# Kernel optimization log

Measured on AMD Instinct MI355X. Metric: run time of the kernel, lower is better.

The kernel has to match this reference:

```python
import jax, jax.numpy as jnp
import numpy as np

N = 20000          # nodes
E = 320000         # edges (avg degree 16)
HID = 256          # hidden_size
HEADS = 8          # num_heads
HD = HID // HEADS  # head_dim = 32


def setup_inputs() -> dict:
    key = jax.random.key(0)
    ks = jax.random.split(key, 12)
    scale = 1.0 / np.sqrt(HID).astype(np.float32)
    def lin_w(k):
        return jax.random.normal(k, (HID, HID), jnp.float32) * scale
    def lin_b(k):
        return jax.random.normal(k, (HID,), jnp.float32) * 0.01
    return {
        "h":   jax.random.normal(ks[0], (N, HID), jnp.float32),
        "Wq": lin_w(ks[1]), "bq": lin_b(ks[2]),
        "Wk": lin_w(ks[3]), "bk": lin_b(ks[4]),
        "Wv": lin_w(ks[5]), "bv": lin_b(ks[6]),
        "Wo": lin_w(ks[7]), "bo": lin_b(ks[8]),
        "rows": jax.random.randint(ks[9],  (E,), 0, N),  # dst/query node of each edge
        "cols": jax.random.randint(ks[10], (E,), 0, N),  # src/key node of each edge
    }


def reference(h, Wq, bq, Wk, bk, Wv, bv, Wo, bo, rows, cols):
    n = h.shape[0]
    scaling = HD ** (-0.5)
    # projections; reshape exactly as torch: (N, head_dim, num_heads)
    q = ((h @ Wq) + bq).reshape(n, HD, HEADS) * scaling
    k = ((h @ Wk) + bk).reshape(n, HD, HEADS)
    v = ((h @ Wv) + bv).reshape(n, HD, HEADS)
    # bsddmm: per-edge, per-head score s[e,h] = sum_d q[rows[e],d,h] * k[cols[e],d,h]
    s = jnp.einsum("edh,edh->eh", q[rows], k[cols])  # [E, HEADS]
    # sparse row-wise softmax (over each row's edges)
    m = jax.ops.segment_max(s, rows, num_segments=n)          # [N, HEADS]
    e = jnp.exp(s - m[rows])                                   # [E, HEADS]
    z = jax.ops.segment_sum(e, rows, num_segments=n)           # [N, HEADS]
    attn = e / z[rows]                                          # [E, HEADS]
    # bspmm: out[i,d,h] = sum_{e: rows[e]=i} attn[e,h] * v[cols[e],d,h]
    out = jax.ops.segment_sum(attn[:, None, :] * v[cols], rows, num_segments=n)  # [N, HD, HEADS]
    return out.reshape(n, -1) @ Wo + bo
```

## Files before the change

### kernel.cpp

```cpp
#include <hip/hip_runtime.h>
#include <hip/hip_bf16.h>
#include <math.h>

#define NNODES 20000
#define NEDGES 320000

using f32x4 = __attribute__((ext_vector_type(4))) float;
using s16x8 = __attribute__((ext_vector_type(8))) short;
using u16x8 = __attribute__((ext_vector_type(8))) unsigned short;

__device__ __forceinline__ float bf2f(unsigned short u) {
    union { unsigned int i; float f; } c; c.i = ((unsigned int)u) << 16; return c.f;
}
__device__ __forceinline__ unsigned short f2bf(float f) {
    __hip_bfloat16 h = __float2bfloat16(f);
    return *reinterpret_cast<unsigned short*>(&h);
}
__device__ __forceinline__ u16x8 packA(const float4& x, const float4& y) {
    u16x8 u; u[0]=f2bf(x.x); u[1]=f2bf(x.y); u[2]=f2bf(x.z); u[3]=f2bf(x.w);
             u[4]=f2bf(y.x); u[5]=f2bf(y.y); u[6]=f2bf(y.z); u[7]=f2bf(y.w);
    return u;
}

__global__ __launch_bounds__(256) void prep_hist_k(
    const float* __restrict__ Wq, const float* __restrict__ bq,
    const float* __restrict__ Wk, const float* __restrict__ bk,
    const float* __restrict__ Wv, const float* __restrict__ bv,
    const float* __restrict__ Wo, const int* __restrict__ rows,
    unsigned short* __restrict__ wt, float* __restrict__ bp,
    int* __restrict__ counts)
{
    const int gid = blockIdx.x * 256 + threadIdx.x;
    const float SC = 0.17677669529663687f;
    if (gid < 262144) {
        const int mat = gid >> 16, r = gid & 65535;
        if (mat < 3) {
            const int k = r >> 8, c = r & 255;
            const int n_old = ((c & 31) << 3) | (c >> 5);
            const float* W = (mat == 0) ? Wq : (mat == 1) ? Wk : Wv;
            float val = W[k * 256 + n_old];
            if (mat == 0) val *= SC;
            wt[mat * 65536 + c * 256 + k] = f2bf(val);
        } else {
            const int c = r >> 8, n = r & 255;
            const int n_old = ((c & 31) << 3) | (c >> 5);
            wt[3 * 65536 + n * 256 + c] = f2bf(Wo[n_old * 256 + n]);
        }
    } else if (gid < 262912) {
        const int idx = gid - 262144;
        const int mat = idx >> 8, c = idx & 255;
        const int n_old = ((c & 31) << 3) | (c >> 5);
        const float* b = (mat == 0) ? bq : (mat == 1) ? bk : bv;
        float val = b[n_old];
        if (mat == 0) val *= SC;
        bp[mat * 256 + c] = val;
    } else if (gid < 262912 + NEDGES) {
        atomicAdd(&counts[rows[gid - 262912]], 1);
    }
}

__global__ __launch_bounds__(1024) void scan_k(const int* __restrict__ counts,
                                               int* __restrict__ row_start)
{
    __shared__ int wsum[16];
    const int t = threadIdx.x, lane = t & 63, w = t >> 6;
    const int base = t * 20;
    int c[20]; int s = 0;
    #pragma unroll
    for (int j = 0; j < 20; ++j) {
        const int idx = base + j;
        c[j] = (idx < NNODES) ? counts[idx] : 0;
        s += c[j];
    }
    int incl = s;
    #pragma unroll
    for (int off = 1; off < 64; off <<= 1) {
        const int y = __shfl_up(incl, off);
        if (lane >= off) incl += y;
    }
    if (lane == 63) wsum[w] = incl;
    __syncthreads();
    int prev = 0;
    for (int i = 0; i < w; ++i) prev += wsum[i];
    int run = prev + incl - s;
    if (t == 0) row_start[0] = 0;
    #pragma unroll
    for (int j = 0; j < 20; ++j) {
        const int idx = base + j;
        run += c[j];
        if (idx < NNODES) row_start[idx + 1] = run;
    }
}

__global__ void scatter_k(const int* __restrict__ rows, const int* __restrict__ cols,
                          const int* __restrict__ row_start, int* __restrict__ cursor,
                          int* __restrict__ cols_sorted)
{
    const int i = blockIdx.x * blockDim.x + threadIdx.x;
    if (i < NEDGES) {
        const int r = rows[i];
        const int pos = row_start[r] + atomicAdd(&cursor[r], 1);
        cols_sorted[pos] = cols[i];
    }
}

__global__ __launch_bounds__(256) void qkv_mfma_k(
    const float* __restrict__ h,
    const unsigned short* __restrict__ wt, const float* __restrict__ bp,
    unsigned short* __restrict__ qo, unsigned short* __restrict__ kv)
{
    const int bm = blockIdx.x * 128;
    const int mat = blockIdx.y >> 1;
    const int bn = (blockIdx.y & 1) * 128;
    const unsigned short* W = wt + mat * 65536;
    const float* bias = bp + mat * 256;

    __shared__ __align__(16) unsigned short As[2][128][40];
    __shared__ __align__(16) unsigned short Bs[2][128][40];

    const int t = threadIdx.x;
    const int lane = t & 63, w = t >> 6;
    const int wr = (w >> 1) * 64, wc = (w & 1) * 64;

    f32x4 acc[4][4];
    #pragma unroll
    for (int i = 0; i < 4; ++i)
        #pragma unroll
        for (int j = 0; j < 4; ++j) acc[i][j] = (f32x4){0.f, 0.f, 0.f, 0.f};

    const int srow = t >> 2, koff = (t & 3) * 8;
    const int m0 = min(bm + srow, NNODES - 1);
    const int m1 = min(bm + srow + 64, NNODES - 1);
    const float* pa0 = h + m0 * 256 + koff;
    const float* pa1 = h + m1 * 256 + koff;
    const unsigned short* pb0 = W + (bn + srow) * 256 + koff;
    const unsigned short* pb1 = W + (bn + srow + 64) * 256 + koff;

    float4 fa0a = *(const float4*)(pa0), fa0b = *(const float4*)(pa0 + 4);
    float4 fa1a = *(const float4*)(pa1), fa1b = *(const float4*)(pa1 + 4);
    u16x8 rb0 = *(const u16x8*)(pb0), rb1 = *(const u16x8*)(pb1);

    *(u16x8*)&As[0][srow][koff]      = packA(fa0a, fa0b);
    *(u16x8*)&As[0][srow + 64][koff] = packA(fa1a, fa1b);
    *(u16x8*)&Bs[0][srow][koff]      = rb0;
    *(u16x8*)&Bs[0][srow + 64][koff] = rb1;
    __syncthreads();

    #pragma unroll
    for (int kt = 0; kt < 8; ++kt) {
        const int cur = kt & 1;
        if (kt < 7) {
            const int k0 = (kt + 1) * 32;
            fa0a = *(const float4*)(pa0 + k0); fa0b = *(const float4*)(pa0 + k0 + 4);
            fa1a = *(const float4*)(pa1 + k0); fa1b = *(const float4*)(pa1 + k0 + 4);
            rb0 = *(const u16x8*)(pb0 + k0);   rb1 = *(const u16x8*)(pb1 + k0);
        }
        s16x8 a[4], b[4];
        const int kk = (lane >> 4) * 8;
        #pragma unroll
        for (int i = 0; i < 4; ++i) {
            a[i] = *(const s16x8*)&As[cur][wr + i * 16 + (lane & 15)][kk];
            b[i] = *(const s16x8*)&Bs[cur][wc + i * 16 + (lane & 15)][kk];
        }
        #pragma unroll
        for (int i = 0; i < 4; ++i)
            #pragma unroll
            for (int j = 0; j < 4; ++j)
                acc[i][j] = __builtin_amdgcn_mfma_f32_16x16x32_bf16(a[i], b[j], acc[i][j], 0, 0, 0);
        if (kt < 7) {
            __syncthreads();
            *(u16x8*)&As[cur ^ 1][srow][koff]      = packA(fa0a, fa0b);
            *(u16x8*)&As[cur ^ 1][srow + 64][koff] = packA(fa1a, fa1b);
            *(u16x8*)&Bs[cur ^ 1][srow][koff]      = rb0;
            *(u16x8*)&Bs[cur ^ 1][srow + 64][koff] = rb1;
            __syncthreads();
        }
    }
    #pragma unroll
    for (int i = 0; i < 4; ++i)
        #pragma unroll
        for (int j = 0; j < 4; ++j) {
            const int n = bn + wc + j * 16 + (lane & 15);
            const float bval = bias[n];
            const int kvbase = ((n >> 2) << 3) + (n & 3) + ((mat == 2) ? 4 : 0);
            #pragma unroll
            for (int r = 0; r < 4; ++r) {
                const int m = bm + wr + i * 16 + (lane >> 4) * 4 + r;
                if (m < NNODES) {
                    const unsigned short val = f2bf(acc[i][j][r] + bval);
                    if (mat == 0) qo[m * 256 + n] = val;
                    else          kv[m * 512 + kvbase] = val;
                }
            }
        }
}

__global__ __launch_bounds__(256) void out_mfma_k(
    const unsigned short* __restrict__ A,
    const unsigned short* __restrict__ wt, const float* __restrict__ bo,
    float* __restrict__ C)
{
    const int bm = blockIdx.x * 128;
    const int bn = blockIdx.y * 128;
    const unsigned short* W = wt + 3 * 65536;

    __shared__ __align__(16) unsigned short As[2][128][40];
    __shared__ __align__(16) unsigned short Bs[2][128][40];

    const int t = threadIdx.x;
    const int lane = t & 63, w = t >> 6;
    const int wr = (w >> 1) * 64, wc = (w & 1) * 64;

    f32x4 acc[4][4];
    #pragma unroll
    for (int i = 0; i < 4; ++i)
        #pragma unroll
        for (int j = 0; j < 4; ++j) acc[i][j] = (f32x4){0.f, 0.f, 0.f, 0.f};

    const int srow = t >> 2, koff = (t & 3) * 8;
    const int m0 = min(bm + srow, NNODES - 1);
    const int m1 = min(bm + srow + 64, NNODES - 1);
    const unsigned short* pa0 = A + m0 * 256 + koff;
    const unsigned short* pa1 = A + m1 * 256 + koff;
    const unsigned short* pb0 = W + (bn + srow) * 256 + koff;
    const unsigned short* pb1 = W + (bn + srow + 64) * 256 + koff;

    u16x8 ra0 = *(const u16x8*)(pa0), ra1 = *(const u16x8*)(pa1);
    u16x8 rb0 = *(const u16x8*)(pb0), rb1 = *(const u16x8*)(pb1);

    *(u16x8*)&As[0][srow][koff]      = ra0;
    *(u16x8*)&As[0][srow + 64][koff] = ra1;
    *(u16x8*)&Bs[0][srow][koff]      = rb0;
    *(u16x8*)&Bs[0][srow + 64][koff] = rb1;
    __syncthreads();

    #pragma unroll
    for (int kt = 0; kt < 8; ++kt) {
        const int cur = kt & 1;
        if (kt < 7) {
            const int k0 = (kt + 1) * 32;
            ra0 = *(const u16x8*)(pa0 + k0); ra1 = *(const u16x8*)(pa1 + k0);
            rb0 = *(const u16x8*)(pb0 + k0); rb1 = *(const u16x8*)(pb1 + k0);
        }
        s16x8 a[4], b[4];
        const int kk = (lane >> 4) * 8;
        #pragma unroll
        for (int i = 0; i < 4; ++i) {
            a[i] = *(const s16x8*)&As[cur][wr + i * 16 + (lane & 15)][kk];
            b[i] = *(const s16x8*)&Bs[cur][wc + i * 16 + (lane & 15)][kk];
        }
        #pragma unroll
        for (int i = 0; i < 4; ++i)
            #pragma unroll
            for (int j = 0; j < 4; ++j)
                acc[i][j] = __builtin_amdgcn_mfma_f32_16x16x32_bf16(a[i], b[j], acc[i][j], 0, 0, 0);
        if (kt < 7) {
            __syncthreads();
            *(u16x8*)&As[cur ^ 1][srow][koff]      = ra0;
            *(u16x8*)&As[cur ^ 1][srow + 64][koff] = ra1;
            *(u16x8*)&Bs[cur ^ 1][srow][koff]      = rb0;
            *(u16x8*)&Bs[cur ^ 1][srow + 64][koff] = rb1;
            __syncthreads();
        }
    }
    #pragma unroll
    for (int i = 0; i < 4; ++i)
        #pragma unroll
        for (int j = 0; j < 4; ++j) {
            const int n = bn + wc + j * 16 + (lane & 15);
            const float bval = bo[n];
            #pragma unroll
            for (int r = 0; r < 4; ++r) {
                const int m = bm + wr + i * 16 + (lane >> 4) * 4 + r;
                if (m < NNODES) C[m * 256 + n] = acc[i][j][r] + bval;
            }
        }
}

__global__ __launch_bounds__(256) void row_attn_k(
    const unsigned short* __restrict__ q, const unsigned short* __restrict__ kv,
    const int* __restrict__ row_start, const int* __restrict__ cols_sorted,
    unsigned short* __restrict__ ot)
{
    const int lane = threadIdx.x & 63;
    const int row = __builtin_amdgcn_readfirstlane(blockIdx.x * 4 + (threadIdx.x >> 6));
    const int rs = row_start[row];
    const int re = row_start[row + 1];
    const int deg = re - rs;

    const ushort4 qu = *reinterpret_cast<const ushort4*>(&q[row * 256 + lane * 4]);
    const float q0 = bf2f(qu.x), q1 = bf2f(qu.y), q2 = bf2f(qu.z), q3 = bf2f(qu.w);
    float z = 0.f, o0 = 0.f, o1 = 0.f, o2 = 0.f, o3 = 0.f;

    const int* cp = cols_sorted + rs;
    for (int i0 = 0; i0 < deg; i0 += 8) {
        u16x8 kvb[8];
        #pragma unroll
        for (int j = 0; j < 8; ++j) {
            const int jj = min(i0 + j, deg - 1);
            const int cn = cp[jj];
            kvb[j] = *reinterpret_cast<const u16x8*>(&kv[cn * 512 + lane * 8]);
        }
        #pragma unroll
        for (int j = 0; j < 8; ++j) {
            float p = q0 * bf2f(kvb[j][0]);
            p = fmaf(q1, bf2f(kvb[j][1]), p);
            p = fmaf(q2, bf2f(kvb[j][2]), p);
            p = fmaf(q3, bf2f(kvb[j][3]), p);
            p += __shfl_xor(p, 1);
            p += __shfl_xor(p, 2);
            p += __shfl_xor(p, 4);
            const float e = (i0 + j < deg) ? __expf(p) : 0.f;
            z += e;
            o0 = fmaf(e, bf2f(kvb[j][4]), o0);
            o1 = fmaf(e, bf2f(kvb[j][5]), o1);
            o2 = fmaf(e, bf2f(kvb[j][6]), o2);
            o3 = fmaf(e, bf2f(kvb[j][7]), o3);
        }
    }
    ushort4 r;
    if (deg > 0) {
        const float iz = 1.0f / z;
        r.x = f2bf(o0 * iz); r.y = f2bf(o1 * iz);
        r.z = f2bf(o2 * iz); r.w = f2bf(o3 * iz);
    } else {
        r.x = r.y = r.z = r.w = 0;
    }
    *reinterpret_cast<ushort4*>(&ot[row * 256 + lane * 4]) = r;
}

extern "C" void kernel_launch(void* const* d_in, const int* in_sizes, int n_in,
                              void* d_out, int out_size, void* d_ws, size_t ws_size,
                              hipStream_t stream)
{
    const float* h  = (const float*)d_in[0];
    const float* Wq = (const float*)d_in[1];
    const float* bq = (const float*)d_in[2];
    const float* Wk = (const float*)d_in[3];
    const float* bk = (const float*)d_in[4];
    const float* Wv = (const float*)d_in[5];
    const float* bv = (const float*)d_in[6];
    const float* Wo = (const float*)d_in[7];
    const float* bo = (const float*)d_in[8];
    const int* rows = (const int*)d_in[9];
    const int* cols = (const int*)d_in[10];
    float* outp = (float*)d_out;

    char* ws = (char*)d_ws;
    unsigned short* q_b  = (unsigned short*)(ws + 0);
    unsigned short* kv_b = (unsigned short*)(ws + 10240000);
    unsigned short* ot_b = (unsigned short*)(ws + 30720000);
    unsigned short* wt   = (unsigned short*)(ws + 40960000);
    float* bp            = (float*)(ws + 41484288);
    int* row_start       = (int*)(ws + 41487360);
    int* counts          = (int*)(ws + 41567488);
    int* cursor          = (int*)(ws + 41647488);
    int* cols_sorted     = (int*)(ws + 41727488);

    hipMemsetAsync(ws + 41567488, 0, 160000, stream);

    prep_hist_k<<<2277, 256, 0, stream>>>(Wq, bq, Wk, bk, Wv, bv, Wo, rows,
                                          wt, bp, counts);
    scan_k<<<1, 1024, 0, stream>>>(counts, row_start);
    scatter_k<<<1250, 256, 0, stream>>>(rows, cols, row_start, cursor, cols_sorted);
    qkv_mfma_k<<<dim3(157, 6), 256, 0, stream>>>(h, wt, bp, q_b, kv_b);
    row_attn_k<<<5000, 256, 0, stream>>>(q_b, kv_b, row_start, cols_sorted, ot_b);
    out_mfma_k<<<dim3(157, 2), 256, 0, stream>>>(ot_b, wt, bo, outp);
}
```

Baseline: 233.2 us.

## Pre-convert h to bf16, shrink GEMM tiles, and restructure row attention

h is now converted to bf16 in the prep kernel rather than inside the QKV GEMM. Both GEMMs move to 64-row tiles with single-buffered LDS, which doubles the number of blocks. The row attention kernel now handles two edges per wavefront, one per 32-lane half, with 8 head dims per lane from an interleaved 16-element K/V layout. It uses software-pipelined loads, DPP reductions, and exp2 with log2e folded into the Q scale. This is meant to raise memory-level parallelism and occupancy, at the cost of an extra h write and read and less GEMM double buffering.

```diff
diff --git a/kernel.cpp b/kernel.cpp
--- a/kernel.cpp
+++ b/kernel.cpp
@@ -16,22 +16,25 @@
     __hip_bfloat16 h = __float2bfloat16(f);
     return *reinterpret_cast<unsigned short*>(&h);
 }
-__device__ __forceinline__ u16x8 packA(const float4& x, const float4& y) {
-    u16x8 u; u[0]=f2bf(x.x); u[1]=f2bf(x.y); u[2]=f2bf(x.z); u[3]=f2bf(x.w);
-             u[4]=f2bf(y.x); u[5]=f2bf(y.y); u[6]=f2bf(y.z); u[7]=f2bf(y.w);
-    return u;
-}
-
-__global__ __launch_bounds__(256) void prep_hist_k(
+template <int CTRL>
+__device__ __forceinline__ float dpp_xadd(float x) {
+    union { float f; int i; } a, b;
+    a.f = x;
+    b.i = __builtin_amdgcn_update_dpp(0, a.i, CTRL, 0xf, 0xf, true);
+    return x + b.f;
+}
+
+__global__ __launch_bounds__(256) void prep_all_k(
     const float* __restrict__ Wq, const float* __restrict__ bq,
     const float* __restrict__ Wk, const float* __restrict__ bk,
     const float* __restrict__ Wv, const float* __restrict__ bv,
     const float* __restrict__ Wo, const int* __restrict__ rows,
+    const float* __restrict__ h,
     unsigned short* __restrict__ wt, float* __restrict__ bp,
-    int* __restrict__ counts)
+    int* __restrict__ counts, unsigned short* __restrict__ hb)
 {
     const int gid = blockIdx.x * 256 + threadIdx.x;
-    const float SC = 0.17677669529663687f;
+    const float SCQ = 0.17677669529663687f * 1.4426950408889634f;
     if (gid < 262144) {
         const int mat = gid >> 16, r = gid & 65535;
         if (mat < 3) {
@@ -39,7 +42,7 @@
             const int n_old = ((c & 31) << 3) | (c >> 5);
             const float* W = (mat == 0) ? Wq : (mat == 1) ? Wk : Wv;
             float val = W[k * 256 + n_old];
-            if (mat == 0) val *= SC;
+            if (mat == 0) val *= SCQ;
             wt[mat * 65536 + c * 256 + k] = f2bf(val);
         } else {
             const int c = r >> 8, n = r & 255;
@@ -52,10 +55,16 @@
         const int n_old = ((c & 31) << 3) | (c >> 5);
         const float* b = (mat == 0) ? bq : (mat == 1) ? bk : bv;
         float val = b[n_old];
-        if (mat == 0) val *= SC;
+        if (mat == 0) val *= SCQ;
         bp[mat * 256 + c] = val;
-    } else if (gid < 262912 + NEDGES) {
+    } else if (gid < 582912) {
         atomicAdd(&counts[rows[gid - 262912]], 1);
+    } else {
+        const int i = (gid - 582912) * 4;
+        const float4 f = *reinterpret_cast<const float4*>(&h[i]);
+        ushort4 u;
+        u.x = f2bf(f.x); u.y = f2bf(f.y); u.z = f2bf(f.z); u.w = f2bf(f.w);
+        *reinterpret_cast<ushort4*>(&hb[i]) = u;
     }
 }
 
@@ -105,84 +114,73 @@
 }
 
 __global__ __launch_bounds__(256) void qkv_mfma_k(
-    const float* __restrict__ h,
+    const unsigned short* __restrict__ hb,
     const unsigned short* __restrict__ wt, const float* __restrict__ bp,
     unsigned short* __restrict__ qo, unsigned short* __restrict__ kv)
 {
-    const int bm = blockIdx.x * 128;
+    const int bm = blockIdx.x * 64;
     const int mat = blockIdx.y >> 1;
     const int bn = (blockIdx.y & 1) * 128;
     const unsigned short* W = wt + mat * 65536;
     const float* bias = bp + mat * 256;
 
-    __shared__ __align__(16) unsigned short As[2][128][40];
-    __shared__ __align__(16) unsigned short Bs[2][128][40];
+    __shared__ __align__(16) unsigned short As[64][40];
+    __shared__ __align__(16) unsigned short Bs[128][40];
 
     const int t = threadIdx.x;
     const int lane = t & 63, w = t >> 6;
-    const int wr = (w >> 1) * 64, wc = (w & 1) * 64;
-
-    f32x4 acc[4][4];
-    #pragma unroll
-    for (int i = 0; i < 4; ++i)
+    const int wr = (w >> 1) * 32, wc = (w & 1) * 64;
+
+    f32x4 acc[2][4];
+    #pragma unroll
+    for (int i = 0; i < 2; ++i)
         #pragma unroll
         for (int j = 0; j < 4; ++j) acc[i][j] = (f32x4){0.f, 0.f, 0.f, 0.f};
 
-    const int srow = t >> 2, koff = (t & 3) * 8;
-    const int m0 = min(bm + srow, NNODES - 1);
-    const int m1 = min(bm + srow + 64, NNODES - 1);
-    const float* pa0 = h + m0 * 256 + koff;
-    const float* pa1 = h + m1 * 256 + koff;
-    const unsigned short* pb0 = W + (bn + srow) * 256 + koff;
-    const unsigned short* pb1 = W + (bn + srow + 64) * 256 + koff;
-
-    float4 fa0a = *(const float4*)(pa0), fa0b = *(const float4*)(pa0 + 4);
-    float4 fa1a = *(const float4*)(pa1), fa1b = *(const float4*)(pa1 + 4);
-    u16x8 rb0 = *(const u16x8*)(pb0), rb1 = *(const u16x8*)(pb1);
-
-    *(u16x8*)&As[0][srow][koff]      = packA(fa0a, fa0b);
-    *(u16x8*)&As[0][srow + 64][koff] = packA(fa1a, fa1b);
-    *(u16x8*)&Bs[0][srow][koff]      = rb0;
-    *(u16x8*)&Bs[0][srow + 64][koff] = rb1;
-    __syncthreads();
+    const int arow = t >> 2, koff = (t & 3) * 8;
+    const int m0 = min(bm + arow, NNODES - 1);
+    const unsigned short* pa  = hb + m0 * 256 + koff;
+    const unsigned short* pb0 = W + (bn + arow) * 256 + koff;
+    const unsigned short* pb1 = W + (bn + arow + 64) * 256 + koff;
+
+    u16x8 ra  = *(const u16x8*)(pa);
+    u16x8 rb0 = *(const u16x8*)(pb0);
+    u16x8 rb1 = *(const u16x8*)(pb1);
 
     #pragma unroll
     for (int kt = 0; kt < 8; ++kt) {
-        const int cur = kt & 1;
+        __syncthreads();
+        *(u16x8*)&As[arow][koff]      = ra;
+        *(u16x8*)&Bs[arow][koff]      = rb0;
+        *(u16x8*)&Bs[arow + 64][koff] = rb1;
+        __syncthreads();
         if (kt < 7) {
             const int k0 = (kt + 1) * 32;
-            fa0a = *(const float4*)(pa0 + k0); fa0b = *(const float4*)(pa0 + k0 + 4);
-            fa1a = *(const float4*)(pa1 + k0); fa1b = *(const float4*)(pa1 + k0 + 4);
-            rb0 = *(const u16x8*)(pb0 + k0);   rb1 = *(const u16x8*)(pb1 + k0);
-        }
-        s16x8 a[4], b[4];
+            ra  = *(const u16x8*)(pa + k0);
+            rb0 = *(const u16x8*)(pb0 + k0);
+            rb1 = *(const u16x8*)(pb1 + k0);
+        }
+        s16x8 a[2], b[4];
         const int kk = (lane >> 4) * 8;
         #pragma unroll
-        for (int i = 0; i < 4; ++i) {
-            a[i] = *(const s16x8*)&As[cur][wr + i * 16 + (lane & 15)][kk];
-            b[i] = *(const s16x8*)&Bs[cur][wc + i * 16 + (lane & 15)][kk];
-        }
-        #pragma unroll
-        for (int i = 0; i < 4; ++i)
+        for (int i = 0; i < 2; ++i)
+            a[i] = *(const s16x8*)&As[wr + i * 16 + (lane & 15)][kk];
+        #pragma unroll
+        for (int j = 0; j < 4; ++j)
+            b[j] = *(const s16x8*)&Bs[wc + j * 16 + (lane & 15)][kk];
+        #pragma unroll
+        for (int i = 0; i < 2; ++i)
             #pragma unroll
             for (int j = 0; j < 4; ++j)
                 acc[i][j] = __builtin_amdgcn_mfma_f32_16x16x32_bf16(a[i], b[j], acc[i][j], 0, 0, 0);
-        if (kt < 7) {
-            __syncthreads();
-            *(u16x8*)&As[cur ^ 1][srow][koff]      = packA(fa0a, fa0b);
-            *(u16x8*)&As[cur ^ 1][srow + 64][koff] = packA(fa1a, fa1b);
-            *(u16x8*)&Bs[cur ^ 1][srow][koff]      = rb0;
-            *(u16x8*)&Bs[cur ^ 1][srow + 64][koff] = rb1;
-            __syncthreads();
-        }
-    }
-    #pragma unroll
-    for (int i = 0; i < 4; ++i)
+    }
+    #pragma unroll
+    for (int i = 0; i < 2; ++i)
         #pragma unroll
         for (int j = 0; j < 4; ++j) {
             const int n = bn + wc + j * 16 + (lane & 15);
             const float bval = bias[n];
-            const int kvbase = ((n >> 2) << 3) + (n & 3) + ((mat == 2) ? 4 : 0);
+            const int kvbase = ((n >> 3) << 4) + (n & 7) + ((mat == 2) ? 8 : 0);
             #pragma unroll
             for (int r = 0; r < 4; ++r) {
                 const int m = bm + wr + i * 16 + (lane >> 4) * 4 + r;
@@ -200,71 +198,62 @@
     const unsigned short* __restrict__ wt, const float* __restrict__ bo,
     float* __restrict__ C)
 {
-    const int bm = blockIdx.x * 128;
+    const int bm = blockIdx.x * 64;
     const int bn = blockIdx.y * 128;
     const unsigned short* W = wt + 3 * 65536;
 
-    __shared__ __align__(16) unsigned short As[2][128][40];
-    __shared__ __align__(16) unsigned short Bs[2][128][40];
+    __shared__ __align__(16) unsigned short As[64][40];
+    __shared__ __align__(16) unsigned short Bs[128][40];
 
     const int t = threadIdx.x;
     const int lane = t & 63, w = t >> 6;
-    const int wr = (w >> 1) * 64, wc = (w & 1) * 64;
-
-    f32x4 acc[4][4];
-    #pragma unroll
-    for (int i = 0; i < 4; ++i)
+    const int wr = (w >> 1) * 32, wc = (w & 1) * 64;
+
+    f32x4 acc[2][4];
+    #pragma unroll
+    for (int i = 0; i < 2; ++i)
         #pragma unroll
         for (int j = 0; j < 4; ++j) acc[i][j] = (f32x4){0.f, 0.f, 0.f, 0.f};
 
-    const int srow = t >> 2, koff = (t & 3) * 8;
-    const int m0 = min(bm + srow, NNODES - 1);
-    const int m1 = min(bm + srow + 64, NNODES - 1);
-    const unsigned short* pa0 = A + m0 * 256 + koff;
-    const unsigned short* pa1 = A + m1 * 256 + koff;
-    const unsigned short* pb0 = W + (bn + srow) * 256 + koff;
-    const unsigned short* pb1 = W + (bn + srow + 64) * 256 + koff;
-
-    u16x8 ra0 = *(const u16x8*)(pa0), ra1 = *(const u16x8*)(pa1);
-    u16x8 rb0 = *(const u16x8*)(pb0), rb1 = *(const u16x8*)(pb1);
-
-    *(u16x8*)&As[0][srow][koff]      = ra0;
-    *(u16x8*)&As[0][srow + 64][koff] = ra1;
-    *(u16x8*)&Bs[0][srow][koff]      = rb0;
-    *(u16x8*)&Bs[0][srow + 64][koff] = rb1;
-    __syncthreads();
+    const int arow = t >> 2, koff = (t & 3) * 8;
+    const int m0 = min(bm + arow, NNODES - 1);
+    const unsigned short* pa  = A + m0 * 256 + koff;
+    const unsigned short* pb0 = W + (bn + arow) * 256 + koff;
+    const unsigned short* pb1 = W + (bn + arow + 64) * 256 + koff;
+
+    u16x8 ra  = *(const u16x8*)(pa);
+    u16x8 rb0 = *(const u16x8*)(pb0);
+    u16x8 rb1 = *(const u16x8*)(pb1);
 
     #pragma unroll
     for (int kt = 0; kt < 8; ++kt) {
-        const int cur = kt & 1;
+        __syncthreads();
+        *(u16x8*)&As[arow][koff]      = ra;
+        *(u16x8*)&Bs[arow][koff]      = rb0;
+        *(u16x8*)&Bs[arow + 64][koff] = rb1;
+        __syncthreads();
         if (kt < 7) {
             const int k0 = (kt + 1) * 32;
-            ra0 = *(const u16x8*)(pa0 + k0); ra1 = *(const u16x8*)(pa1 + k0);
-            rb0 = *(const u16x8*)(pb0 + k0); rb1 = *(const u16x8*)(pb1 + k0);
-        }
-        s16x8 a[4], b[4];
+            ra  = *(const u16x8*)(pa + k0);
+            rb0 = *(const u16x8*)(pb0 + k0);
+            rb1 = *(const u16x8*)(pb1 + k0);
+        }
+        s16x8 a[2], b[4];
         const int kk = (lane >> 4) * 8;
         #pragma unroll
-        for (int i = 0; i < 4; ++i) {
-            a[i] = *(const s16x8*)&As[cur][wr + i * 16 + (lane & 15)][kk];
-            b[i] = *(const s16x8*)&Bs[cur][wc + i * 16 + (lane & 15)][kk];
-        }
-        #pragma unroll
-        for (int i = 0; i < 4; ++i)
+        for (int i = 0; i < 2; ++i)
+            a[i] = *(const s16x8*)&As[wr + i * 16 + (lane & 15)][kk];
+        #pragma unroll
+        for (int j = 0; j < 4; ++j)
+            b[j] = *(const s16x8*)&Bs[wc + j * 16 + (lane & 15)][kk];
+        #pragma unroll
+        for (int i = 0; i < 2; ++i)
             #pragma unroll
             for (int j = 0; j < 4; ++j)
                 acc[i][j] = __builtin_amdgcn_mfma_f32_16x16x32_bf16(a[i], b[j], acc[i][j], 0, 0, 0);
-        if (kt < 7) {
-            __syncthreads();
-            *(u16x8*)&As[cur ^ 1][srow][koff]      = ra0;
-            *(u16x8*)&As[cur ^ 1][srow + 64][koff] = ra1;
-            *(u16x8*)&Bs[cur ^ 1][srow][koff]      = rb0;
-            *(u16x8*)&Bs[cur ^ 1][srow + 64][koff] = rb1;
-            __syncthreads();
-        }
-    }
-    #pragma unroll
-    for (int i = 0; i < 4; ++i)
+    }
+    #pragma unroll
+    for (int i = 0; i < 2; ++i)
         #pragma unroll
         for (int j = 0; j < 4; ++j) {
             const int n = bn + wc + j * 16 + (lane & 15);
@@ -283,50 +272,88 @@
     unsigned short* __restrict__ ot)
 {
     const int lane = threadIdx.x & 63;
+    const int w5 = lane & 31;
+    const int half = lane >> 5;
     const int row = __builtin_amdgcn_readfirstlane(blockIdx.x * 4 + (threadIdx.x >> 6));
     const int rs = row_start[row];
     const int re = row_start[row + 1];
     const int deg = re - rs;
 
-    const ushort4 qu = *reinterpret_cast<const ushort4*>(&q[row * 256 + lane * 4]);
-    const float q0 = bf2f(qu.x), q1 = bf2f(qu.y), q2 = bf2f(qu.z), q3 = bf2f(qu.w);
-    float z = 0.f, o0 = 0.f, o1 = 0.f, o2 = 0.f, o3 = 0.f;
-
+    float qd[8];
+    {
+        const u16x8 qu = *reinterpret_cast<const u16x8*>(&q[row * 256 + w5 * 8]);
+        #pragma unroll
+        for (int d = 0; d < 8; ++d) qd[d] = bf2f(qu[d]);
+    }
+    float o[8] = {0.f, 0.f, 0.f, 0.f, 0.f, 0.f, 0.f, 0.f};
+    float z = 0.f;
     const int* cp = cols_sorted + rs;
-    for (int i0 = 0; i0 < deg; i0 += 8) {
-        u16x8 kvb[8];
-        #pragma unroll
-        for (int j = 0; j < 8; ++j) {
-            const int jj = min(i0 + j, deg - 1);
-            const int cn = cp[jj];
-            kvb[j] = *reinterpret_cast<const u16x8*>(&kv[cn * 512 + lane * 8]);
-        }
-        #pragma unroll
-        for (int j = 0; j < 8; ++j) {
-            float p = q0 * bf2f(kvb[j][0]);
-            p = fmaf(q1, bf2f(kvb[j][1]), p);
-            p = fmaf(q2, bf2f(kvb[j][2]), p);
-            p = fmaf(q3, bf2f(kvb[j][3]), p);
-            p += __shfl_xor(p, 1);
-            p += __shfl_xor(p, 2);
-            p += __shfl_xor(p, 4);
-            const float e = (i0 + j < deg) ? __expf(p) : 0.f;
-            z += e;
-            o0 = fmaf(e, bf2f(kvb[j][4]), o0);
-            o1 = fmaf(e, bf2f(kvb[j][5]), o1);
-            o2 = fmaf(e, bf2f(kvb[j][6]), o2);
-            o3 = fmaf(e, bf2f(kvb[j][7]), o3);
-        }
-    }
-    ushort4 r;
+
+#define LP(K, V, base) do { \
+    const int c0 = cp[min((base), deg - 1)]; \
+    const int c1 = cp[min((base) + 1, deg - 1)]; \
+    const int cn = half ? c1 : c0; \
+    const unsigned short* p_ = kv + cn * 512 + w5 * 16; \
+    K = *reinterpret_cast<const u16x8*>(p_); \
+    V = *reinterpret_cast<const u16x8*>(p_ + 8); \
+} while (0)
+
+#define CMP(K, V, base) do { \
+    float pa_ = qd[0] * bf2f(K[0]); \
+    float pb_ = qd[1] * bf2f(K[1]); \
+    pa_ = fmaf(qd[2], bf2f(K[2]), pa_); \
+    pb_ = fmaf(qd[3], bf2f(K[3]), pb_); \
+    pa_ = fmaf(qd[4], bf2f(K[4]), pa_); \
+    pb_ = fmaf(qd[5], bf2f(K[5]), pb_); \
+    pa_ = fmaf(qd[6], bf2f(K[6]), pa_); \
+    pb_ = fmaf(qd[7], bf2f(K[7]), pb_); \
+    float p_ = pa_ + pb_; \
+    p_ = dpp_xadd<0xB1>(p_); \
+    p_ = dpp_xadd<0x4E>(p_); \
+    const float e_ = ((base) + half < deg) ? exp2f(p_) : 0.f; \
+    z += e_; \
+    o[0] = fmaf(e_, bf2f(V[0]), o[0]); \
+    o[1] = fmaf(e_, bf2f(V[1]), o[1]); \
+    o[2] = fmaf(e_, bf2f(V[2]), o[2]); \
+    o[3] = fmaf(e_, bf2f(V[3]), o[3]); \
+    o[4] = fmaf(e_, bf2f(V[4]), o[4]); \
+    o[5] = fmaf(e_, bf2f(V[5]), o[5]); \
+    o[6] = fmaf(e_, bf2f(V[6]), o[6]); \
+    o[7] = fmaf(e_, bf2f(V[7]), o[7]); \
+} while (0)
+
     if (deg > 0) {
-        const float iz = 1.0f / z;
-        r.x = f2bf(o0 * iz); r.y = f2bf(o1 * iz);
-        r.z = f2bf(o2 * iz); r.w = f2bf(o3 * iz);
-    } else {
-        r.x = r.y = r.z = r.w = 0;
-    }
-    *reinterpret_cast<ushort4*>(&ot[row * 256 + lane * 4]) = r;
+        u16x8 ak0, av0, ak1, av1, bk0, bv0, bk1, bv1;
+        LP(ak0, av0, 0);
+        LP(ak1, av1, 2);
+        for (int i0 = 0; i0 < deg; i0 += 8) {
+            const bool hb = (i0 + 4) < deg;
+            if (hb) { LP(bk0, bv0, i0 + 4); LP(bk1, bv1, i0 + 6); }
+            CMP(ak0, av0, i0);
+            CMP(ak1, av1, i0 + 2);
+            if (i0 + 8 < deg) { LP(ak0, av0, i0 + 8); LP(ak1, av1, i0 + 10); }
+            if (hb) { CMP(bk0, bv0, i0 + 4); CMP(bk1, bv1, i0 + 6); }
+        }
+    }
+#undef LP
+#undef CMP
+
+    z += __shfl_xor(z, 32);
+    #pragma unroll
+    for (int d = 0; d < 8; ++d) o[d] += __shfl_xor(o[d], 32);
+
+    if (half == 0) {
+        u16x8 r;
+        if (deg > 0) {
+            const float iz = 1.0f / z;
+            #pragma unroll
+            for (int d = 0; d < 8; ++d) r[d] = f2bf(o[d] * iz);
+        } else {
+            #pragma unroll
+            for (int d = 0; d < 8; ++d) r[d] = 0;
+        }
+        *reinterpret_cast<u16x8*>(&ot[row * 256 + w5 * 8]) = r;
+    }
 }
 
 extern "C" void kernel_launch(void* const* d_in, const int* in_sizes, int n_in,
@@ -350,20 +377,21 @@
     unsigned short* q_b  = (unsigned short*)(ws + 0);
     unsigned short* kv_b = (unsigned short*)(ws + 10240000);
     unsigned short* ot_b = (unsigned short*)(ws + 30720000);
-    unsigned short* wt   = (unsigned short*)(ws + 40960000);
-    float* bp            = (float*)(ws + 41484288);
-    int* row_start       = (int*)(ws + 41487360);
-    int* counts          = (int*)(ws + 41567488);
-    int* cursor          = (int*)(ws + 41647488);
-    int* cols_sorted     = (int*)(ws + 41727488);
-
-    hipMemsetAsync(ws + 41567488, 0, 160000, stream);
-
-    prep_hist_k<<<2277, 256, 0, stream>>>(Wq, bq, Wk, bk, Wv, bv, Wo, rows,
-                                          wt, bp, counts);
+    unsigned short* h_b  = (unsigned short*)(ws + 40960000);
+    unsigned short* wt   = (unsigned short*)(ws + 51200000);
+    float* bp            = (float*)(ws + 51724288);
+    int* row_start       = (int*)(ws + 51727360);
+    int* counts          = (int*)(ws + 51807488);
+    int* cursor          = (int*)(ws + 51887488);
+    int* cols_sorted     = (int*)(ws + 51967488);
+
+    hipMemsetAsync(ws + 51807488, 0, 160000, stream);
+
+    prep_all_k<<<7277, 256, 0, stream>>>(Wq, bq, Wk, bk, Wv, bv, Wo, rows, h,
+                                         wt, bp, counts, h_b);
     scan_k<<<1, 1024, 0, stream>>>(counts, row_start);
     scatter_k<<<1250, 256, 0, stream>>>(rows, cols, row_start, cursor, cols_sorted);
-    qkv_mfma_k<<<dim3(157, 6), 256, 0, stream>>>(h, wt, bp, q_b, kv_b);
+    qkv_mfma_k<<<dim3(313, 6), 256, 0, stream>>>(h_b, wt, bp, q_b, kv_b);
     row_attn_k<<<5000, 256, 0, stream>>>(q_b, kv_b, row_start, cols_sorted, ot_b);
-    out_mfma_k<<<dim3(157, 2), 256, 0, stream>>>(ot_b, wt, bo, outp);
-}
+    out_mfma_k<<<dim3(313, 2), 256, 0, stream>>>(ot_b, wt, bo, outp);
+}
```

Measured after the change: 222.9 us. -4.4%, faster.
